# Optimization experiments

Hardware: AMD Instinct MI355X
Metric: run time of the kernel (lower is better)

The kernel has to match this reference:

```python
import jax, jax.numpy as jnp
import numpy as np

N_NODES = 100000
D = 128
N_EDGES = 500000
EPS = 1e-05


def setup_inputs() -> dict:
    key = jax.random.key(0)
    k1, k2, k3 = jax.random.split(key, 3)
    embed = jax.random.uniform(k1, (N_NODES, D), dtype=jnp.float32)
    weight = jax.random.uniform(k2, (N_EDGES, 1), dtype=jnp.float32)
    edge_idx = jax.random.randint(k3, (N_EDGES, 2), 0, N_NODES, dtype=jnp.int64)
    return {"embed": embed, "weight": weight, "edge_idx": edge_idx}


def reference(embed, weight, edge_idx):
    # Original math: sigmoid(log((A @ B.T) @ w) + 1e-5)
    # where A = embed[edge_idx[:,0]] (E,d), B = embed[edge_idx[:,1]] (E,d), w (E,1).
    # Reassociate (A @ B.T) @ w == A @ (B.T @ w) to avoid the ExE intermediate.
    A = embed[edge_idx[:, 0]]                 # (E, d) gather
    B = embed[edge_idx[:, 1]]                 # (E, d) gather
    btw = jnp.einsum('ed,eo->do', B, weight)  # (d, 1)  tiny contraction
    score = A @ btw                           # (E, 1)
    return jax.nn.sigmoid(jnp.log(score) + EPS)
```

## Files before the change

kernel.cpp:

```cpp
#include <hip/hip_runtime.h>

#define D 128
#define EPS 1e-5f
#define SCAN_ROWS 8
#define HW_PER_BLK 8

__global__ __launch_bounds__(256) void zero_kernel(
    float4* __restrict__ p, int n4)
{
    const int i = blockIdx.x * blockDim.x + threadIdx.x;
    if (i < n4) p[i] = {0.f, 0.f, 0.f, 0.f};
}

__global__ __launch_bounds__(256) void wsum_kernel(
    const float* __restrict__ weight,
    const int* __restrict__ eidx,
    float* __restrict__ wsum,
    int nEdges)
{
    const int t = blockIdx.x * blockDim.x + threadIdx.x;
    const int e0 = 2 * t;
    if (e0 + 1 < nEdges) {
        const int4   p = reinterpret_cast<const int4*>(eidx)[t];
        const float2 w = reinterpret_cast<const float2*>(weight)[t];
        unsafeAtomicAdd(&wsum[p.y], w.x);
        unsafeAtomicAdd(&wsum[p.w], w.y);
    } else if (e0 < nEdges) {
        unsafeAtomicAdd(&wsum[eidx[2 * e0 + 1]], weight[e0]);
    }
}

__global__ __launch_bounds__(256, 8) void btw_partial_kernel(
    const float* __restrict__ embed,
    const float* __restrict__ wsum,
    float* __restrict__ partialT,
    int nNodes, int nScanBlk)
{
    __shared__ float sbtw[D];
    const int tid = threadIdx.x;
    for (int i = tid; i < D; i += 256) sbtw[i] = 0.f;
    __syncthreads();

    const int j  = tid & 31;
    const int hw = blockIdx.x * HW_PER_BLK + (tid >> 5);
    const int n0 = hw * SCAN_ROWS;

    float4 acc = {0.f, 0.f, 0.f, 0.f};
    if (n0 + SCAN_ROWS <= nNodes) {
        float4 v[SCAN_ROWS];
        float  w[SCAN_ROWS];
        #pragma unroll
        for (int r = 0; r < SCAN_ROWS; ++r)
            v[r] = reinterpret_cast<const float4*>(embed + (size_t)(n0 + r) * D)[j];
        #pragma unroll
        for (int r = 0; r < SCAN_ROWS; ++r)
            w[r] = wsum[n0 + r];
        #pragma unroll
        for (int r = 0; r < SCAN_ROWS; ++r) {
            acc.x += w[r] * v[r].x;
            acc.y += w[r] * v[r].y;
            acc.z += w[r] * v[r].z;
            acc.w += w[r] * v[r].w;
        }
    } else {
        for (int r = 0; r < SCAN_ROWS && n0 + r < nNodes; ++r) {
            const float  w = wsum[n0 + r];
            const float4 v = reinterpret_cast<const float4*>(embed + (size_t)(n0 + r) * D)[j];
            acc.x += w * v.x; acc.y += w * v.y; acc.z += w * v.z; acc.w += w * v.w;
        }
    }

    atomicAdd(&sbtw[4*j+0], acc.x);
    atomicAdd(&sbtw[4*j+1], acc.y);
    atomicAdd(&sbtw[4*j+2], acc.z);
    atomicAdd(&sbtw[4*j+3], acc.w);
    __syncthreads();
    if (tid < D) partialT[(size_t)tid * nScanBlk + blockIdx.x] = sbtw[tid];
}

__global__ __launch_bounds__(256) void btw_reduce_kernel(
    const float* __restrict__ partialT,
    float* __restrict__ btw,
    int nScanBlk)
{
    __shared__ float red[256];
    const int d = blockIdx.x;
    const int tid = threadIdx.x;
    float s = 0.f;
    const float* row = partialT + (size_t)d * nScanBlk;
    for (int k = tid; k < nScanBlk; k += 256) s += row[k];
    red[tid] = s;
    __syncthreads();
    for (int off = 128; off > 0; off >>= 1) {
        if (tid < off) red[tid] += red[tid + off];
        __syncthreads();
    }
    if (tid == 0) btw[d] = red[0];
}

__global__ __launch_bounds__(256, 8) void snode_kernel(
    const float* __restrict__ embed,
    const float* __restrict__ btw,
    float* __restrict__ snode,
    int nNodes)
{
    const int tid = threadIdx.x;
    const int j = tid & 31;
    const float4 bt = reinterpret_cast<const float4*>(btw)[j];
    const int hw = blockIdx.x * HW_PER_BLK + (tid >> 5);
    const int n0 = hw * SCAN_ROWS;

    if (n0 + SCAN_ROWS <= nNodes) {
        float4 v[SCAN_ROWS];
        #pragma unroll
        for (int r = 0; r < SCAN_ROWS; ++r)
            v[r] = reinterpret_cast<const float4*>(embed + (size_t)(n0 + r) * D)[j];
        float s[SCAN_ROWS];
        #pragma unroll
        for (int r = 0; r < SCAN_ROWS; ++r)
            s[r] = v[r].x*bt.x + v[r].y*bt.y + v[r].z*bt.z + v[r].w*bt.w;
        #pragma unroll
        for (int m = 1; m < 32; m <<= 1) {
            #pragma unroll
            for (int r = 0; r < SCAN_ROWS; ++r)
                s[r] += __shfl_xor(s[r], m, 64);
        }
        if (j == 0) {
            float4 o0 = {s[0], s[1], s[2], s[3]};
            float4 o1 = {s[4], s[5], s[6], s[7]};
            reinterpret_cast<float4*>(snode + n0)[0] = o0;
            reinterpret_cast<float4*>(snode + n0)[1] = o1;
        }
    } else if (n0 < nNodes) {
        for (int r = 0; r < SCAN_ROWS && n0 + r < nNodes; ++r) {
            const float4 v = reinterpret_cast<const float4*>(embed + (size_t)(n0 + r) * D)[j];
            float s = v.x*bt.x + v.y*bt.y + v.z*bt.z + v.w*bt.w;
            #pragma unroll
            for (int m = 1; m < 32; m <<= 1) s += __shfl_xor(s, m, 64);
            if (j == 0) snode[n0 + r] = s;
        }
    }
}

__global__ __launch_bounds__(256) void out_kernel(
    const int* __restrict__ eidx,
    const float* __restrict__ snode,
    float* __restrict__ out,
    int nEdges)
{
    const float c = 0.9999900000499999f;
    const int t = blockIdx.x * blockDim.x + threadIdx.x;
    const int e0 = 2 * t;
    if (e0 + 1 < nEdges) {
        const int4 p = reinterpret_cast<const int4*>(eidx)[t];
        const float sa = snode[p.x];
        const float sb = snode[p.z];
        float2 o = { sa / (sa + c), sb / (sb + c) };
        reinterpret_cast<float2*>(out)[t] = o;
    } else if (e0 < nEdges) {
        const float s = snode[eidx[2 * e0]];
        out[e0] = s / (s + c);
    }
}

extern "C" void kernel_launch(void* const* d_in, const int* in_sizes, int n_in,
                              void* d_out, int out_size, void* d_ws, size_t ws_size,
                              hipStream_t stream) {
    const float* embed  = (const float*)d_in[0];
    const float* weight = (const float*)d_in[1];
    const int*   eidx   = (const int*)d_in[2];
    float* out = (float*)d_out;

    const int nEdges = in_sizes[1];
    const int nNodes = in_sizes[0] / D;

    float* wsum     = (float*)d_ws;
    float* btw      = wsum + nNodes;
    float* snode    = btw + D;
    float* partialT = snode + nNodes;

    const int nZero4   = (nNodes + 3) / 4;
    const int zBlocks  = (nZero4 + 255) / 256;
    const int pBlocks  = ((nEdges + 1) / 2 + 255) / 256;
    const int nScanBlk = (nNodes + SCAN_ROWS * HW_PER_BLK - 1) / (SCAN_ROWS * HW_PER_BLK);

    zero_kernel       <<<zBlocks,  256, 0, stream>>>((float4*)d_ws, nZero4);
    wsum_kernel       <<<pBlocks,  256, 0, stream>>>(weight, eidx, wsum, nEdges);
    btw_partial_kernel<<<nScanBlk, 256, 0, stream>>>(embed, wsum, partialT, nNodes, nScanBlk);
    btw_reduce_kernel <<<D,        256, 0, stream>>>(partialT, btw, nScanBlk);
    snode_kernel      <<<nScanBlk, 256, 0, stream>>>(embed, btw, snode, nNodes);
    out_kernel        <<<pBlocks,  256, 0, stream>>>(eidx, snode, out, nEdges);
}
```

Measured before the change: 67.54 us.

## Replace btw reduce kernel with padded global atomics; process four edges per thread

Each scan block now atomically adds its 128-wide partial of B^T w straight into a zeroed global array, padded to one slot per 16 floats, and the separate reduce kernel and partial buffer are dropped. The zero kernel is extended to clear the padded array, and snode reads the strided values. The wsum and out kernels each handle four edges per thread, with wider index and weight loads. The aim is to save a launch and the partial-buffer round trip, at the cost of about 1,563 blocks contending on 128 atomic addresses and a nondeterministic summation order.

New measurement: 94.98 us. 40.6% more time.

```diff
diff --git a/kernel.cpp b/kernel.cpp
--- a/kernel.cpp
+++ b/kernel.cpp
@@ -4,6 +4,7 @@
 #define EPS 1e-5f
 #define SCAN_ROWS 8
 #define HW_PER_BLK 8
+#define PAD 16
 
 __global__ __launch_bounds__(256) void zero_kernel(
     float4* __restrict__ p, int n4)
@@ -19,22 +20,26 @@
     int nEdges)
 {
     const int t = blockIdx.x * blockDim.x + threadIdx.x;
-    const int e0 = 2 * t;
-    if (e0 + 1 < nEdges) {
-        const int4   p = reinterpret_cast<const int4*>(eidx)[t];
-        const float2 w = reinterpret_cast<const float2*>(weight)[t];
-        unsafeAtomicAdd(&wsum[p.y], w.x);
-        unsafeAtomicAdd(&wsum[p.w], w.y);
-    } else if (e0 < nEdges) {
-        unsafeAtomicAdd(&wsum[eidx[2 * e0 + 1]], weight[e0]);
+    const int e0 = 4 * t;
+    if (e0 + 3 < nEdges) {
+        const int4 p0 = reinterpret_cast<const int4*>(eidx)[2 * t];
+        const int4 p1 = reinterpret_cast<const int4*>(eidx)[2 * t + 1];
+        const float4 w = reinterpret_cast<const float4*>(weight)[t];
+        unsafeAtomicAdd(&wsum[p0.y], w.x);
+        unsafeAtomicAdd(&wsum[p0.w], w.y);
+        unsafeAtomicAdd(&wsum[p1.y], w.z);
+        unsafeAtomicAdd(&wsum[p1.w], w.w);
+    } else {
+        for (int e = e0; e < nEdges; ++e)
+            unsafeAtomicAdd(&wsum[eidx[2 * e + 1]], weight[e]);
     }
 }
 
 __global__ __launch_bounds__(256, 8) void btw_partial_kernel(
     const float* __restrict__ embed,
     const float* __restrict__ wsum,
-    float* __restrict__ partialT,
-    int nNodes, int nScanBlk)
+    float* __restrict__ btwPad,
+    int nNodes)
 {
     __shared__ float sbtw[D];
     const int tid = threadIdx.x;
@@ -75,38 +80,19 @@
     atomicAdd(&sbtw[4*j+2], acc.z);
     atomicAdd(&sbtw[4*j+3], acc.w);
     __syncthreads();
-    if (tid < D) partialT[(size_t)tid * nScanBlk + blockIdx.x] = sbtw[tid];
-}
-
-__global__ __launch_bounds__(256) void btw_reduce_kernel(
-    const float* __restrict__ partialT,
-    float* __restrict__ btw,
-    int nScanBlk)
-{
-    __shared__ float red[256];
-    const int d = blockIdx.x;
-    const int tid = threadIdx.x;
-    float s = 0.f;
-    const float* row = partialT + (size_t)d * nScanBlk;
-    for (int k = tid; k < nScanBlk; k += 256) s += row[k];
-    red[tid] = s;
-    __syncthreads();
-    for (int off = 128; off > 0; off >>= 1) {
-        if (tid < off) red[tid] += red[tid + off];
-        __syncthreads();
-    }
-    if (tid == 0) btw[d] = red[0];
+    if (tid < D) unsafeAtomicAdd(&btwPad[tid * PAD], sbtw[tid]);
 }
 
 __global__ __launch_bounds__(256, 8) void snode_kernel(
     const float* __restrict__ embed,
-    const float* __restrict__ btw,
+    const float* __restrict__ btwPad,
     float* __restrict__ snode,
     int nNodes)
 {
     const int tid = threadIdx.x;
     const int j = tid & 31;
-    const float4 bt = reinterpret_cast<const float4*>(btw)[j];
+    const float4 bt = { btwPad[(4*j+0) * PAD], btwPad[(4*j+1) * PAD],
+                        btwPad[(4*j+2) * PAD], btwPad[(4*j+3) * PAD] };
     const int hw = blockIdx.x * HW_PER_BLK + (tid >> 5);
     const int n0 = hw * SCAN_ROWS;
 
@@ -150,16 +136,22 @@
 {
     const float c = 0.9999900000499999f;
     const int t = blockIdx.x * blockDim.x + threadIdx.x;
-    const int e0 = 2 * t;
-    if (e0 + 1 < nEdges) {
-        const int4 p = reinterpret_cast<const int4*>(eidx)[t];
-        const float sa = snode[p.x];
-        const float sb = snode[p.z];
-        float2 o = { sa / (sa + c), sb / (sb + c) };
-        reinterpret_cast<float2*>(out)[t] = o;
-    } else if (e0 < nEdges) {
-        const float s = snode[eidx[2 * e0]];
-        out[e0] = s / (s + c);
+    const int e0 = 4 * t;
+    if (e0 + 3 < nEdges) {
+        const int4 p0 = reinterpret_cast<const int4*>(eidx)[2 * t];
+        const int4 p1 = reinterpret_cast<const int4*>(eidx)[2 * t + 1];
+        const float s0 = snode[p0.x];
+        const float s1 = snode[p0.z];
+        const float s2 = snode[p1.x];
+        const float s3 = snode[p1.z];
+        float4 o = { s0 / (s0 + c), s1 / (s1 + c),
+                     s2 / (s2 + c), s3 / (s3 + c) };
+        reinterpret_cast<float4*>(out)[t] = o;
+    } else {
+        for (int e = e0; e < nEdges; ++e) {
+            const float s = snode[eidx[2 * e]];
+            out[e] = s / (s + c);
+        }
     }
 }
 
@@ -174,20 +166,18 @@
     const int nEdges = in_sizes[1];
     const int nNodes = in_sizes[0] / D;
 
-    float* wsum     = (float*)d_ws;
-    float* btw      = wsum + nNodes;
-    float* snode    = btw + D;
-    float* partialT = snode + nNodes;
+    float* wsum   = (float*)d_ws;
+    float* btwPad = wsum + nNodes;
+    float* snode  = btwPad + D * PAD;
 
-    const int nZero4   = (nNodes + 3) / 4;
+    const int nZero4   = (nNodes + D * PAD + 3) / 4;
     const int zBlocks  = (nZero4 + 255) / 256;
-    const int pBlocks  = ((nEdges + 1) / 2 + 255) / 256;
+    const int eBlocks4 = ((nEdges + 3) / 4 + 255) / 256;
     const int nScanBlk = (nNodes + SCAN_ROWS * HW_PER_BLK - 1) / (SCAN_ROWS * HW_PER_BLK);
 
     zero_kernel       <<<zBlocks,  256, 0, stream>>>((float4*)d_ws, nZero4);
-    wsum_kernel       <<<pBlocks,  256, 0, stream>>>(weight, eidx, wsum, nEdges);
-    btw_partial_kernel<<<nScanBlk, 256, 0, stream>>>(embed, wsum, partialT, nNodes, nScanBlk);
-    btw_reduce_kernel <<<D,        256, 0, stream>>>(partialT, btw, nScanBlk);
-    snode_kernel      <<<nScanBlk, 256, 0, stream>>>(embed, btw, snode, nNodes);
-    out_kernel        <<<pBlocks,  256, 0, stream>>>(eidx, snode, out, nEdges);
+    wsum_kernel       <<<eBlocks4, 256, 0, stream>>>(weight, eidx, wsum, nEdges);
+    btw_partial_kernel<<<nScanBlk, 256, 0, stream>>>(embed, wsum, btwPad, nNodes);
+    snode_kernel      <<<nScanBlk, 256, 0, stream>>>(embed, btwPad, snode, nNodes);
+    out_kernel        <<<eBlocks4, 256, 0, stream>>>(eidx, snode, out, nEdges);
 }
```
